# Optimization experiments

Measured on AMD Instinct MI355X. Metric: run time of the kernel, lower is better.

The kernel has to match this reference:

```python
import jax, jax.numpy as jnp
import numpy as np
from jax import lax

B, N, HID = 2, 2048, 2048
H, KVH, D = 16, 4, 128           # heads, kv heads, head_dim
GROUPS = H // KVH
FLA_WEIGHT = 0.01
NEG = -1e30


def setup_inputs() -> dict:
    key = jax.random.key(0)
    ks = jax.random.split(key, 5)
    s = 0.02
    return {
        "hidden_states": jax.random.normal(ks[0], (B, N, HID), jnp.float32),
        "Wq": jax.random.normal(ks[1], (HID, H * D), jnp.float32) * s,
        "Wk": jax.random.normal(ks[2], (HID, KVH * D), jnp.float32) * s,
        "Wv": jax.random.normal(ks[3], (HID, KVH * D), jnp.float32) * s,
        "Wo": jax.random.normal(ks[4], (H * D, HID), jnp.float32) * s,
    }


def _split_heads(x, h):
    b, n, _ = x.shape
    return x.reshape(b, n, h, -1).transpose(0, 2, 1, 3)  # b h n d


def _gla_attention(q, k, v, scale):
    # Gated linear attention: S_t = sigmoid(k_t) (.) S_{t-1} + k_t (x) v_t,
    # o_t = scale * q_t . S_t ; sequential recurrence over the seq dim.
    qs = jnp.moveaxis(q, 2, 0)  # n b h d
    ks = jnp.moveaxis(k, 2, 0)
    vs = jnp.moveaxis(v, 2, 0)

    def step(S, inp):
        qt, kt, vt = inp                                   # each (b,h,d)
        g = jax.nn.sigmoid(kt)                             # per-key-dim gate
        S = S * g[..., None] + kt[..., None] * vt[..., None, :]  # (b,h,d,dv)
        ot = scale * jnp.einsum('bhd,bhde->bhe', qt, S)
        return S, ot

    S0 = jnp.zeros(q.shape[:2] + (q.shape[-1], v.shape[-1]), q.dtype)
    _, o = lax.scan(step, S0, (qs, ks, vs))                # n b h dv
    return jnp.moveaxis(o, 0, 2)                           # b h n dv


def reference(hidden_states, Wq, Wk, Wv, Wo):
    scale = 1.0 / np.sqrt(D)
    q = _split_heads(hidden_states @ Wq, H)                # b h n d
    k = _split_heads(hidden_states @ Wk, KVH)
    v = _split_heads(hidden_states @ Wv, KVH)
    k = jnp.repeat(k, GROUPS, axis=1)                      # repeat_kv -> b H n d
    v = jnp.repeat(v, GROUPS, axis=1)

    # FLA branch
    fla = _gla_attention(q, k, v, scale)                   # b h n d
    fla = fla.transpose(0, 2, 1, 3).reshape(B, N, H * D)   # b n (h d)

    # Base causal softmax attention
    scores = jnp.einsum('bhnd,bhmd->bhnm', q, k) * scale
    causal = jnp.tril(jnp.ones((N, N), bool))
    scores = jnp.where(causal, scores, NEG)
    attn = jax.nn.softmax(scores, axis=-1)
    base = jnp.einsum('bhnm,bhmd->bhnd', attn, v)
    base = base.transpose(0, 2, 1, 3).reshape(B, N, H * D) @ Wo

    return base + FLA_WEIGHT * fla
```

## Files before the change

### kernel.cpp

```cpp
#include <hip/hip_runtime.h>
#include <hip/hip_bf16.h>
#include <cstdint>
#include <cstddef>


typedef __attribute__((ext_vector_type(4))) float f32x4;
typedef __attribute__((ext_vector_type(2))) float f32x2;
typedef __attribute__((ext_vector_type(8))) short s16x8;
typedef unsigned short u16;
typedef unsigned int u32;

__device__ __forceinline__ float bfu2f(u16 u) {
  union { unsigned int i; float f; } x; x.i = ((unsigned int)u) << 16; return x.f;
}
__device__ __forceinline__ u16 f2bfu(float f) {
  union { float f; unsigned int i; } x; x.f = f;
  unsigned int r = x.i + 0x7fffu + ((x.i >> 16) & 1u);
  return (u16)(r >> 16);
}
__device__ __forceinline__ void bf8_to_f(s16x8 v, float* o) {
  union { s16x8 v; u16 u[8]; } x; x.v = v;
#pragma unroll
  for (int j = 0; j < 8; j++) o[j] = bfu2f(x.u[j]);
}
__device__ __forceinline__ s16x8 pack_bf8(f32x4 lo, f32x4 hi) {
  union { s16x8 v; u16 u[8]; } x;
#pragma unroll
  for (int j = 0; j < 4; j++) { x.u[j] = f2bfu(lo[j]); x.u[4 + j] = f2bfu(hi[j]); }
  return x.v;
}
__device__ __forceinline__ void gload_lds16(const u16* g, u16* l) {
  __builtin_amdgcn_global_load_lds(
      (__attribute__((address_space(1))) void*)(g),
      (__attribute__((address_space(3))) void*)(l), 16, 0, 0);
}

__global__ __launch_bounds__(256) void f32_to_bf16(
    const float* __restrict__ src, u16* __restrict__ dst, int n8) {
  const int i = blockIdx.x * 256 + threadIdx.x;
  if (i < n8) {
    f32x4 a = *(const f32x4*)(src + (size_t)i * 8);
    f32x4 b = *(const f32x4*)(src + (size_t)i * 8 + 4);
    *(s16x8*)(dst + (size_t)i * 8) = pack_bf8(a, b);
  }
}

__global__ __launch_bounds__(256) void transpose_f32_bf16(
    const float* __restrict__ src, u16* __restrict__ dst, int R, int C) {
  __shared__ u16 tile[32][33];
  const int bx = blockIdx.x * 32, by = blockIdx.y * 32;
  const int tx = threadIdx.x & 31, ty = threadIdx.x >> 5;
#pragma unroll
  for (int i = 0; i < 32; i += 8)
    tile[ty + i][tx] = f2bfu(src[(size_t)(by + ty + i) * C + bx + tx]);
  __syncthreads();
#pragma unroll
  for (int i = 0; i < 32; i += 8)
    dst[(size_t)(bx + ty + i) * R + by + tx] = tile[tx][ty + i];
}

__global__ __launch_bounds__(256) void transpose_bf16(
    const u16* __restrict__ src, u16* __restrict__ dst, int R, int C) {
  __shared__ u16 tile[32][33];
  const int bx = blockIdx.x * 32, by = blockIdx.y * 32;
  const int tx = threadIdx.x & 31, ty = threadIdx.x >> 5;
#pragma unroll
  for (int i = 0; i < 32; i += 8)
    tile[ty + i][tx] = src[(size_t)(by + ty + i) * C + bx + tx];
  __syncthreads();
#pragma unroll
  for (int i = 0; i < 32; i += 8)
    dst[(size_t)(bx + ty + i) * R + by + tx] = tile[tx][ty + i];
}

__global__ __launch_bounds__(256) void gemm_t(
    const u16* __restrict__ A, const u16* __restrict__ Bt0, const u16* __restrict__ Bt1,
    u16* __restrict__ Cb0, u16* __restrict__ Cb1, float* __restrict__ Cf,
    int M, int N, int K, const u16* __restrict__ addsrc, float addw) {
  __shared__ u16 Al[128 * 32];
  __shared__ u16 Bl[128 * 32];
  const u16* Bt = blockIdx.z ? Bt1 : Bt0;
  u16* Cb = blockIdx.z ? Cb1 : Cb0;
  const int m0 = blockIdx.y * 128, n0 = blockIdx.x * 128;
  const int t = threadIdx.x, w = t >> 6, l = t & 63, lm = l & 15, lq = l >> 4;
  const int wr = w >> 1, wc = w & 1;
  const f32x4 z4 = {0.f, 0.f, 0.f, 0.f};
  f32x4 acc[4][4];
#pragma unroll
  for (int i = 0; i < 4; i++)
#pragma unroll
    for (int j = 0; j < 4; j++) acc[i][j] = z4;
  const int srow = l >> 2, scol = (l & 3) * 8;
  const u16* Ag = A + (size_t)(m0 + w * 32 + srow) * K + scol;
  const u16* Bg = Bt + (size_t)(n0 + w * 32 + srow) * K + scol;
  u16* Alw = &Al[(w * 32) * 32];
  u16* Blw = &Bl[(w * 32) * 32];
  for (int kk = 0; kk < K; kk += 32) {
    gload_lds16(Ag + kk, Alw);
    gload_lds16(Ag + (size_t)16 * K + kk, Alw + 16 * 32);
    gload_lds16(Bg + kk, Blw);
    gload_lds16(Bg + (size_t)16 * K + kk, Blw + 16 * 32);
    __syncthreads();
    s16x8 af[4], bfr[4];
#pragma unroll
    for (int sm = 0; sm < 4; sm++) af[sm] = *(const s16x8*)&Al[(wr * 64 + sm * 16 + lm) * 32 + lq * 8];
#pragma unroll
    for (int sn = 0; sn < 4; sn++) bfr[sn] = *(const s16x8*)&Bl[(wc * 64 + sn * 16 + lm) * 32 + lq * 8];
#pragma unroll
    for (int sm = 0; sm < 4; sm++)
#pragma unroll
      for (int sn = 0; sn < 4; sn++)
        acc[sm][sn] = __builtin_amdgcn_mfma_f32_16x16x32_bf16(af[sm], bfr[sn], acc[sm][sn], 0, 0, 0);
    __syncthreads();
  }
#pragma unroll
  for (int sm = 0; sm < 4; sm++)
#pragma unroll
    for (int sn = 0; sn < 4; sn++)
#pragma unroll
      for (int r = 0; r < 4; r++) {
        const int row = m0 + wr * 64 + sm * 16 + lq * 4 + r;
        const int col = n0 + wc * 64 + sn * 16 + lm;
        float v = acc[sm][sn][r];
        if (Cf) {
          if (addsrc) v += addw * bfu2f(addsrc[(size_t)row * N + col]);
          Cf[(size_t)row * N + col] = v;
        } else {
          Cb[(size_t)row * N + col] = f2bfu(v);
        }
      }
}

__global__ __launch_bounds__(256) void gemm_qkv(
    const u16* __restrict__ A, const u16* __restrict__ WqT, const u16* __restrict__ WkT,
    const u16* __restrict__ WvT, u16* __restrict__ Qo, u16* __restrict__ Ko,
    u16* __restrict__ Vo) {
  __shared__ u16 Al[128 * 32];
  __shared__ u16 Bl[128 * 32];
  const int bx = blockIdx.x;
  const u16* Bt; u16* Cb; int n0, Nst;
  if (bx < 16)      { Bt = WqT; Cb = Qo; n0 = bx * 128;        Nst = 2048; }
  else if (bx < 20) { Bt = WkT; Cb = Ko; n0 = (bx - 16) * 128; Nst = 512; }
  else              { Bt = WvT; Cb = Vo; n0 = (bx - 20) * 128; Nst = 512; }
  const int K = 2048;
  const int m0 = blockIdx.y * 128;
  const int t = threadIdx.x, w = t >> 6, l = t & 63, lm = l & 15, lq = l >> 4;
  const int wr = w >> 1, wc = w & 1;
  const f32x4 z4 = {0.f, 0.f, 0.f, 0.f};
  f32x4 acc[4][4];
#pragma unroll
  for (int i = 0; i < 4; i++)
#pragma unroll
    for (int j = 0; j < 4; j++) acc[i][j] = z4;
  const int srow = l >> 2, scol = (l & 3) * 8;
  const u16* Ag = A + (size_t)(m0 + w * 32 + srow) * K + scol;
  const u16* Bg = Bt + (size_t)(n0 + w * 32 + srow) * K + scol;
  u16* Alw = &Al[(w * 32) * 32];
  u16* Blw = &Bl[(w * 32) * 32];
  for (int kk = 0; kk < K; kk += 32) {
    gload_lds16(Ag + kk, Alw);
    gload_lds16(Ag + (size_t)16 * K + kk, Alw + 16 * 32);
    gload_lds16(Bg + kk, Blw);
    gload_lds16(Bg + (size_t)16 * K + kk, Blw + 16 * 32);
    __syncthreads();
    s16x8 af[4], bfr[4];
#pragma unroll
    for (int sm = 0; sm < 4; sm++) af[sm] = *(const s16x8*)&Al[(wr * 64 + sm * 16 + lm) * 32 + lq * 8];
#pragma unroll
    for (int sn = 0; sn < 4; sn++) bfr[sn] = *(const s16x8*)&Bl[(wc * 64 + sn * 16 + lm) * 32 + lq * 8];
#pragma unroll
    for (int sm = 0; sm < 4; sm++)
#pragma unroll
      for (int sn = 0; sn < 4; sn++)
        acc[sm][sn] = __builtin_amdgcn_mfma_f32_16x16x32_bf16(af[sm], bfr[sn], acc[sm][sn], 0, 0, 0);
    __syncthreads();
  }
#pragma unroll
  for (int sm = 0; sm < 4; sm++)
#pragma unroll
    for (int sn = 0; sn < 4; sn++)
#pragma unroll
      for (int r = 0; r < 4; r++) {
        const int row = m0 + wr * 64 + sm * 16 + lq * 4 + r;
        const int col = n0 + wc * 64 + sn * 16 + lm;
        Cb[(size_t)row * Nst + col] = f2bfu(acc[sm][sn][r]);
      }
}

__global__ __launch_bounds__(512) void flash_attn_wave(
    const u16* __restrict__ Q, const u16* __restrict__ Kx,
    const u16* __restrict__ Vt, u16* __restrict__ AO) {
  __shared__ u16 Klds[2][64 * 128];
  __shared__ u16 Vlds[2][128 * 64];
  __shared__ u16 Pl[8][16][68];
  const int bid = blockIdx.x;
  const int set = bid & 7;
  const int b = set >> 2, kvh = set & 3;
  const int rest = bid >> 3;
  const int j0 = rest >> 1, hp = rest & 1;
  const int t = threadIdx.x, w = t >> 6, l = t & 63, lm = l & 15, lq = l >> 4;
  const int h = kvh * 4 + hp * 2 + (w & 1);
  const int cs = (w >> 1) & 1, mh = w >> 2;
  const float scale = 0.0883883476483184f;
  const u16* Kbase = Kx + (size_t)(b * 2048) * 512 + kvh * 128;
  const u16* Vbase = Vt + (size_t)(b * 512 + kvh * 128) * 2048;
  const f32x4 z4 = {0.f, 0.f, 0.f, 0.f};

  const int kdst0 = w * 512, kdst1 = 4096 + w * 512;
  const int krow_a = (l >> 4), kcol_sw = (((l & 15) * 16)) >> 1;
  (void)krow_a; (void)kcol_sw;

  auto stage = [&](int kt, int bufi) {
    const int key0 = kt * 64;
#pragma unroll
    for (int r = 0; r < 2; r++) {
      const int row = r * 32 + w * 4 + (l >> 4);
      const int scb = ((l & 15) * 16) ^ ((row & 7) << 4);
      gload_lds16(Kbase + (size_t)(key0 + row) * 512 + (scb >> 1),
                  &Klds[bufi][r * 4096 + w * 512]);
    }
#pragma unroll
    for (int r = 0; r < 2; r++) {
      const int row = r * 64 + w * 8 + (l >> 3);
      const int scb = ((l & 7) * 16) ^ ((row & 7) << 4);
      gload_lds16(Vbase + (size_t)row * 2048 + key0 + (scb >> 1),
                  &Vlds[bufi][r * 4096 + w * 512]);
    }
  };

#pragma unroll 1
  for (int ph = 0; ph < 2; ph++) {
    const int j = ph ? (31 - j0) : j0;
    const int c = 2 * j + cs;
    const int base = c * 32;
    int cur = 0;
    stage(0, 0);
    s16x8 qf[4];
#pragma unroll
    for (int kk = 0; kk < 4; kk++)
      qf[kk] = *(const s16x8*)(Q + ((size_t)(b * 2048 + base + mh * 16 + lm)) * 2048 +
                               h * 128 + kk * 32 + lq * 8);
    f32x4 oacc[8];
#pragma unroll
    for (int e = 0; e < 8; e++) oacc[e] = z4;
    float lsum[4] = {0.f, 0.f, 0.f, 0.f};
#pragma unroll 1
    for (int kt = 0; kt <= j; kt++) {
      const int key0 = kt * 64;
      if (kt < j) {
        stage(kt + 1, cur ^ 1);
        asm volatile("s_waitcnt vmcnt(4)" ::: "memory");
      } else {
        asm volatile("s_waitcnt vmcnt(0)" ::: "memory");
      }
      __builtin_amdgcn_s_barrier();
      const char* KB = (const char*)&Klds[cur][0];
      const char* VB = (const char*)&Vlds[cur][0];
      s16x8 kf[4][4];
#pragma unroll
      for (int nst = 0; nst < 4; nst++)
#pragma unroll
        for (int kk = 0; kk < 4; kk++) {
          const int row = nst * 16 + lm;
          const int cb = (kk * 64 + lq * 16) ^ ((row & 7) << 4);
          kf[nst][kk] = *(const s16x8*)(KB + row * 256 + cb);
        }
      f32x4 sacc[4];
#pragma unroll
      for (int i = 0; i < 4; i++) sacc[i] = z4;
#pragma unroll
      for (int nst = 0; nst < 4; nst++)
#pragma unroll
        for (int kk = 0; kk < 4; kk++)
          sacc[nst] = __builtin_amdgcn_mfma_f32_16x16x32_bf16(
              qf[kk], kf[nst][kk], sacc[nst], 0, 0, 0);
      const bool diag = (kt == j);
#pragma unroll
      for (int r = 0; r < 4; r++) {
        const int qrow = base + mh * 16 + lq * 4 + r;
#pragma unroll
        for (int nst = 0; nst < 4; nst++) {
          float pv = __expf(sacc[nst][r] * scale);
          if (diag && (key0 + nst * 16 + lm > qrow)) pv = 0.f;
          lsum[r] += pv;
          Pl[w][lq * 4 + r][nst * 16 + lm] = f2bfu(pv);
        }
      }
      s16x8 vf[8][2];
#pragma unroll
      for (int et = 0; et < 8; et++)
#pragma unroll
        for (int kc = 0; kc < 2; kc++) {
          const int row = et * 16 + lm;
          const int cb = (kc * 64 + lq * 16) ^ ((row & 7) << 4);
          vf[et][kc] = *(const s16x8*)(VB + row * 128 + cb);
        }
      s16x8 pf[2];
#pragma unroll
      for (int kc = 0; kc < 2; kc++)
        pf[kc] = *(const s16x8*)&Pl[w][lm][kc * 32 + lq * 8];
#pragma unroll
      for (int et = 0; et < 8; et++)
#pragma unroll
        for (int kc = 0; kc < 2; kc++)
          oacc[et] = __builtin_amdgcn_mfma_f32_16x16x32_bf16(
              pf[kc], vf[et][kc], oacc[et], 0, 0, 0);
      asm volatile("s_waitcnt lgkmcnt(0)" ::: "memory");
      __builtin_amdgcn_s_barrier();
      cur ^= 1;
    }
#pragma unroll
    for (int r = 0; r < 4; r++) {
#pragma unroll
      for (int off = 1; off < 16; off <<= 1)
        lsum[r] += __shfl_xor(lsum[r], off, 64);
    }
#pragma unroll
    for (int r = 0; r < 4; r++) {
      const float inv = 1.f / lsum[r];
      const int row = base + mh * 16 + lq * 4 + r;
      u16* op = AO + ((size_t)(b * 2048 + row)) * 2048 + h * 128;
#pragma unroll
      for (int et = 0; et < 8; et++) op[et * 16 + lm] = f2bfu(oacc[et][r] * inv);
    }
  }
}

__global__ __launch_bounds__(256) void fla_contrib32(
    const u16* __restrict__ Kx, const u16* __restrict__ Vt,
    u16* __restrict__ Gg, u16* __restrict__ Ktg, u16* __restrict__ MT,
    float* __restrict__ Lam) {
  __shared__ float gl[32][132];
  __shared__ float kl[32][132];
  __shared__ float ktl[32][132];
  __shared__ u16 khT[128][40];
  const int c = blockIdx.x, kvh = blockIdx.y, b = blockIdx.z;
  const int bk = b * 4 + kvh;
  const int t = threadIdx.x;
  const size_t cb = (size_t)bk * 64 + c;
  {
    const int r = t >> 3, c0 = (t & 7) * 16;
    const u16* kp = Kx + ((size_t)(b * 2048 + c * 32 + r)) * 512 + kvh * 128 + c0;
#pragma unroll
    for (int i = 0; i < 2; i++) {
      float kv[8];
      bf8_to_f(*(const s16x8*)(kp + i * 8), kv);
#pragma unroll
      for (int j = 0; j < 8; j++) {
        kl[r][c0 + i * 8 + j] = kv[j];
        gl[r][c0 + i * 8 + j] = 1.f / (1.f + __expf(-kv[j]));
      }
    }
  }
  __syncthreads();
  if (t < 128) {
    float G = 1.f;
#pragma unroll
    for (int s = 0; s < 32; s++) {
      G *= gl[s][t];
      gl[s][t] = G;
      ktl[s][t] = kl[s][t] / G;
    }
    Lam[cb * 128 + t] = G;
    const float lam = G;
#pragma unroll
    for (int s = 0; s < 32; s++) khT[t][s] = f2bfu(ktl[s][t] * lam);
  }
  __syncthreads();
  {
    const int r = t >> 3, c0 = (t & 7) * 16;
    u16* gp = Gg + cb * 4096 + r * 128 + c0;
    u16* kp = Ktg + cb * 4096 + r * 128 + c0;
#pragma unroll
    for (int i = 0; i < 2; i++) {
      f32x4 a = *(f32x4*)&gl[r][c0 + i * 8];
      f32x4 b2 = *(f32x4*)&gl[r][c0 + i * 8 + 4];
      *(s16x8*)(gp + i * 8) = pack_bf8(a, b2);
      a = *(f32x4*)&ktl[r][c0 + i * 8];
      b2 = *(f32x4*)&ktl[r][c0 + i * 8 + 4];
      *(s16x8*)(kp + i * 8) = pack_bf8(a, b2);
    }
  }
  const int w = t >> 6, l = t & 63, lm = l & 15, lq = l >> 4;
  const f32x4 z4 = {0.f, 0.f, 0.f, 0.f};
  f32x4 macc[2][8];
#pragma unroll
  for (int ei = 0; ei < 2; ei++)
#pragma unroll
    for (int dt = 0; dt < 8; dt++) macc[ei][dt] = z4;
  s16x8 vtf[2];
#pragma unroll
  for (int ei = 0; ei < 2; ei++) {
    const int et = w * 2 + ei;
    vtf[ei] = *(const s16x8*)(Vt + ((size_t)(b * 512 + kvh * 128 + et * 16 + lm)) * 2048 +
                              c * 32 + lq * 8);
  }
#pragma unroll
  for (int dt = 0; dt < 8; dt++) {
    s16x8 kf = *(const s16x8*)&khT[dt * 16 + lm][lq * 8];
#pragma unroll
    for (int ei = 0; ei < 2; ei++)
      macc[ei][dt] = __builtin_amdgcn_mfma_f32_16x16x32_bf16(vtf[ei], kf, macc[ei][dt], 0, 0, 0);
  }
  u16* mp = MT + cb * 16384;
#pragma unroll
  for (int ei = 0; ei < 2; ei++)
#pragma unroll
    for (int dt = 0; dt < 8; dt++)
#pragma unroll
      for (int r = 0; r < 4; r++)
        mp[(size_t)((w * 2 + ei) * 16 + lq * 4 + r) * 128 + dt * 16 + lm] =
            f2bfu(macc[ei][dt][r]);
}

__global__ __launch_bounds__(256) void fla_prefix32(
    const u16* __restrict__ MT, const float* __restrict__ Lam, u16* __restrict__ SwsT) {
  const int eg = blockIdx.x, bk = blockIdx.y;
  const int t = threadIdx.x;
  const int e = eg * 4 + (t >> 6), d0 = (t & 63) * 2;
  const size_t cb0 = (size_t)bk * 64;
  const u16* mp = MT + cb0 * 16384 + e * 128 + d0;
  const float* lp = Lam + cb0 * 128 + d0;
  u16* sp = SwsT + cb0 * 16384 + e * 128 + d0;
  float s0 = 0.f, s1 = 0.f;
  u32 mnext = *(const u32*)mp;
  f32x2 lnext = *(const f32x2*)lp;
#pragma unroll 1
  for (int c = 0; c < 64; c++) {
    const u32 mcur = mnext;
    const f32x2 lcur = lnext;
    if (c < 63) {
      mnext = *(const u32*)(mp + (size_t)(c + 1) * 16384);
      lnext = *(const f32x2*)(lp + (size_t)(c + 1) * 128);
    }
    *(u32*)(sp + (size_t)c * 16384) = (u32)f2bfu(s0) | ((u32)f2bfu(s1) << 16);
    s0 = s0 * lcur[0] + bfu2f((u16)(mcur & 0xffffu));
    s1 = s1 * lcur[1] + bfu2f((u16)(mcur >> 16));
  }
}

__global__ __launch_bounds__(256) void fla_output_mfma(
    const u16* __restrict__ Q, const u16* __restrict__ Gg, const u16* __restrict__ Ktg,
    const u16* __restrict__ SwsT, const u16* __restrict__ Vt, u16* __restrict__ Fla) {
  __shared__ u16 Pl[4][2][16][40];
  const int c = blockIdx.x, h = blockIdx.y, b = blockIdx.z;
  const int kvh = h >> 2, bk = b * 4 + kvh;
  const int t = threadIdx.x, w = t >> 6, l = t & 63, lm = l & 15, lq = l >> 4;
  const float scale = 0.0883883476483184f;
  const size_t cb = (size_t)bk * 64 + c;
  const f32x4 z4 = {0.f, 0.f, 0.f, 0.f};
  s16x8 qgf[2][4];
#pragma unroll
  for (int m = 0; m < 2; m++)
#pragma unroll
    for (int kk = 0; kk < 4; kk++) {
      float qv[8], gv[8];
      bf8_to_f(*(const s16x8*)(Q + ((size_t)(b * 2048 + c * 32 + m * 16 + lm)) * 2048 +
                               h * 128 + kk * 32 + lq * 8), qv);
      bf8_to_f(*(const s16x8*)(Gg + cb * 4096 + (m * 16 + lm) * 128 + kk * 32 + lq * 8), gv);
      f32x4 a, b2;
#pragma unroll
      for (int j = 0; j < 4; j++) { a[j] = qv[j] * gv[j]; b2[j] = qv[4 + j] * gv[4 + j]; }
      qgf[m][kk] = pack_bf8(a, b2);
    }
  f32x4 sacc[2][2];
#pragma unroll
  for (int m = 0; m < 2; m++)
#pragma unroll
    for (int st = 0; st < 2; st++) sacc[m][st] = z4;
#pragma unroll
  for (int st = 0; st < 2; st++)
#pragma unroll
    for (int kk = 0; kk < 4; kk++) {
      s16x8 ktf = *(const s16x8*)(Ktg + cb * 4096 + (st * 16 + lm) * 128 + kk * 32 + lq * 8);
#pragma unroll
      for (int m = 0; m < 2; m++)
        sacc[m][st] = __builtin_amdgcn_mfma_f32_16x16x32_bf16(qgf[m][kk], ktf, sacc[m][st], 0, 0, 0);
    }
#pragma unroll
  for (int m = 0; m < 2; m++)
#pragma unroll
    for (int st = 0; st < 2; st++)
#pragma unroll
      for (int r = 0; r < 4; r++) {
        const int trow = m * 16 + lq * 4 + r;
        const int scol = st * 16 + lm;
        Pl[w][m][lq * 4 + r][st * 16 + lm] = f2bfu(scol <= trow ? sacc[m][st][r] : 0.f);
      }
  s16x8 pf[2];
#pragma unroll
  for (int m = 0; m < 2; m++) pf[m] = *(const s16x8*)&Pl[w][m][lm][lq * 8];
  f32x4 oacc[2][2];
#pragma unroll
  for (int m = 0; m < 2; m++)
#pragma unroll
    for (int ei = 0; ei < 2; ei++) oacc[m][ei] = z4;
#pragma unroll
  for (int ei = 0; ei < 2; ei++) {
    const int et = w * 2 + ei;
    s16x8 vtf = *(const s16x8*)(Vt + ((size_t)(b * 512 + kvh * 128 + et * 16 + lm)) * 2048 +
                                c * 32 + lq * 8);
#pragma unroll
    for (int m = 0; m < 2; m++)
      oacc[m][ei] = __builtin_amdgcn_mfma_f32_16x16x32_bf16(pf[m], vtf, oacc[m][ei], 0, 0, 0);
#pragma unroll
    for (int kk = 0; kk < 4; kk++) {
      s16x8 s0f = *(const s16x8*)(SwsT + cb * 16384 + (et * 16 + lm) * 128 + kk * 32 + lq * 8);
#pragma unroll
      for (int m = 0; m < 2; m++)
        oacc[m][ei] = __builtin_amdgcn_mfma_f32_16x16x32_bf16(qgf[m][kk], s0f, oacc[m][ei], 0, 0, 0);
    }
  }
#pragma unroll
  for (int m = 0; m < 2; m++)
#pragma unroll
    for (int ei = 0; ei < 2; ei++)
#pragma unroll
      for (int r = 0; r < 4; r++)
        Fla[((size_t)(b * 2048 + c * 32 + m * 16 + lq * 4 + r)) * 2048 + h * 128 +
            (w * 2 + ei) * 16 + lm] = f2bfu(scale * oacc[m][ei][r]);
}

extern "C" void kernel_launch(void* const* d_in, const int* in_sizes, int n_in,
                              void* d_out, int out_size, void* d_ws, size_t ws_size,
                              hipStream_t stream) {
  const float* X  = (const float*)d_in[0];
  const float* Wq = (const float*)d_in[1];
  const float* Wk = (const float*)d_in[2];
  const float* Wv = (const float*)d_in[3];
  const float* Wo = (const float*)d_in[4];
  float* out = (float*)d_out;

  char* ws = (char*)d_ws;
  size_t off = 0;
  auto alloc = [&](size_t bytes) { void* p = ws + off; off += (bytes + 255) & ~(size_t)255; return p; };
  u16* WoT = (u16*)alloc(2048ull * 2048 * 2);
  u16* Qb  = (u16*)alloc(4096ull * 2048 * 2);
  u16* Kb  = (u16*)alloc(4096ull * 512 * 2);
  u16* Vb  = (u16*)alloc(4096ull * 512 * 2);
  u16* Vtb = (u16*)alloc(2ull * 512 * 2048 * 2);
  u16* Fla = (u16*)alloc(4096ull * 2048 * 2);
  u16* SH16 = (u16*)alloc(4096ull * 2048 * 2);
  u16* Xb = SH16;
  u16* MT = SH16;
  u16* AO = SH16;
  char* BIG = (char*)alloc(26ull * 1024 * 1024);
  u16* WqT = (u16*)BIG;
  u16* WkT = (u16*)(BIG + 8ull * 1024 * 1024);
  u16* WvT = (u16*)(BIG + 10ull * 1024 * 1024);
  u16* Gg   = (u16*)BIG;
  u16* Ktg  = (u16*)(BIG + 4194304ull);
  u16* SwsT = (u16*)(BIG + 8388608ull);
  float* Lam = (float*)(BIG + 8388608ull + 16777216ull);
  (void)ws_size; (void)in_sizes; (void)n_in; (void)out_size;

  dim3 blk(256);
  f32_to_bf16<<<dim3(4096), blk, 0, stream>>>(X, Xb, 4096 * 2048 / 8);
  transpose_f32_bf16<<<dim3(64, 64), blk, 0, stream>>>(Wq, WqT, 2048, 2048);
  transpose_f32_bf16<<<dim3(16, 64), blk, 0, stream>>>(Wk, WkT, 2048, 512);
  transpose_f32_bf16<<<dim3(16, 64), blk, 0, stream>>>(Wv, WvT, 2048, 512);
  transpose_f32_bf16<<<dim3(64, 64), blk, 0, stream>>>(Wo, WoT, 2048, 2048);

  gemm_qkv<<<dim3(24, 32), blk, 0, stream>>>(Xb, WqT, WkT, WvT, Qb, Kb, Vb);

  transpose_bf16<<<dim3(16, 64), blk, 0, stream>>>(Vb, Vtb, 2048, 512);
  transpose_bf16<<<dim3(16, 64), blk, 0, stream>>>(Vb + 2048ull * 512, Vtb + 512ull * 2048, 2048, 512);

  fla_contrib32<<<dim3(64, 4, 2), blk, 0, stream>>>(Kb, Vtb, Gg, Ktg, MT, Lam);
  fla_prefix32<<<dim3(32, 8), blk, 0, stream>>>(MT, Lam, SwsT);
  fla_output_mfma<<<dim3(64, 16, 2), blk, 0, stream>>>(Qb, Gg, Ktg, SwsT, Vtb, Fla);

  flash_attn_wave<<<dim3(256), dim3(512), 0, stream>>>(Qb, Kb, Vtb, AO);

  gemm_t<<<dim3(16, 32, 1), blk, 0, stream>>>(AO, WoT, WoT, nullptr, nullptr, out,
                                              4096, 2048, 2048, Fla, 0.01f);
}
```

Before: 384.7 us.

## Rewrite QKV and output GEMMs with double-buffered 256x128 tiles and swizzled LDS

Result: slower. 396.6 us (+3.1%).

```diff
diff --git a/kernel.cpp b/kernel.cpp
--- a/kernel.cpp
+++ b/kernel.cpp
@@ -73,45 +73,81 @@
     dst[(size_t)(bx + ty + i) * R + by + tx] = tile[tx][ty + i];
 }
 
-__global__ __launch_bounds__(256) void gemm_t(
-    const u16* __restrict__ A, const u16* __restrict__ Bt0, const u16* __restrict__ Bt1,
-    u16* __restrict__ Cb0, u16* __restrict__ Cb1, float* __restrict__ Cf,
-    int M, int N, int K, const u16* __restrict__ addsrc, float addw) {
-  __shared__ u16 Al[128 * 32];
-  __shared__ u16 Bl[128 * 32];
-  const u16* Bt = blockIdx.z ? Bt1 : Bt0;
-  u16* Cb = blockIdx.z ? Cb1 : Cb0;
-  const int m0 = blockIdx.y * 128, n0 = blockIdx.x * 128;
+__device__ __forceinline__ void gemm_core_256x128(
+    const u16* __restrict__ A, const u16* __restrict__ Bt,
+    int m0, int n0, int K, int Nst,
+    u16* __restrict__ Cb, float* __restrict__ Cf,
+    const u16* __restrict__ addsrc, float addw,
+    u16* Abuf, u16* Bbuf) {
   const int t = threadIdx.x, w = t >> 6, l = t & 63, lm = l & 15, lq = l >> 4;
   const int wr = w >> 1, wc = w & 1;
+  const int tr = t >> 3, tc8 = (t & 7) * 8;
   const f32x4 z4 = {0.f, 0.f, 0.f, 0.f};
   f32x4 acc[4][4];
 #pragma unroll
   for (int i = 0; i < 4; i++)
 #pragma unroll
     for (int j = 0; j < 4; j++) acc[i][j] = z4;
-  const int srow = l >> 2, scol = (l & 3) * 8;
-  const u16* Ag = A + (size_t)(m0 + w * 32 + srow) * K + scol;
-  const u16* Bg = Bt + (size_t)(n0 + w * 32 + srow) * K + scol;
-  u16* Alw = &Al[(w * 32) * 32];
-  u16* Blw = &Bl[(w * 32) * 32];
-  for (int kk = 0; kk < K; kk += 32) {
-    gload_lds16(Ag + kk, Alw);
-    gload_lds16(Ag + (size_t)16 * K + kk, Alw + 16 * 32);
-    gload_lds16(Bg + kk, Blw);
-    gload_lds16(Bg + (size_t)16 * K + kk, Blw + 16 * 32);
-    __syncthreads();
-    s16x8 af[4], bfr[4];
-#pragma unroll
-    for (int sm = 0; sm < 4; sm++) af[sm] = *(const s16x8*)&Al[(wr * 64 + sm * 16 + lm) * 32 + lq * 8];
-#pragma unroll
-    for (int sn = 0; sn < 4; sn++) bfr[sn] = *(const s16x8*)&Bl[(wc * 64 + sn * 16 + lm) * 32 + lq * 8];
-#pragma unroll
-    for (int sm = 0; sm < 4; sm++)
-#pragma unroll
-      for (int sn = 0; sn < 4; sn++)
-        acc[sm][sn] = __builtin_amdgcn_mfma_f32_16x16x32_bf16(af[sm], bfr[sn], acc[sm][sn], 0, 0, 0);
-    __syncthreads();
+  const u16* Ag = A + (size_t)m0 * K;
+  const u16* Bg = Bt + (size_t)n0 * K;
+  auto stage = [&](int kt, int bufi) {
+#pragma unroll
+    for (int i = 0; i < 4; i++) {
+      const int row = i * 64 + tr;
+      const int col = tc8 ^ ((row & 7) << 3);
+      gload_lds16(Ag + (size_t)row * K + kt * 64 + col,
+                  Abuf + bufi * 16384 + i * 4096 + w * 512);
+    }
+#pragma unroll
+    for (int i = 0; i < 2; i++) {
+      const int row = i * 64 + tr;
+      const int col = tc8 ^ ((row & 7) << 3);
+      gload_lds16(Bg + (size_t)row * K + kt * 64 + col,
+                  Bbuf + bufi * 8192 + i * 4096 + w * 512);
+    }
+  };
+  const int nt = K >> 6;
+  stage(0, 0);
+  int cur = 0;
+#pragma unroll 1
+  for (int kt = 0; kt < nt; kt++) {
+    if (kt + 1 < nt) {
+      stage(kt + 1, cur ^ 1);
+      asm volatile("s_waitcnt vmcnt(6)" ::: "memory");
+    } else {
+      asm volatile("s_waitcnt vmcnt(0)" ::: "memory");
+    }
+    __builtin_amdgcn_s_barrier();
+    const u16* Ab = Abuf + cur * 16384;
+    const u16* Bb = Bbuf + cur * 8192;
+    s16x8 af[4][2], bff[4][2];
+#pragma unroll
+    for (int sm = 0; sm < 4; sm++) {
+      const int row = wr * 64 + sm * 16 + lm;
+#pragma unroll
+      for (int kk = 0; kk < 2; kk++)
+        af[sm][kk] = *(const s16x8*)&Ab[row * 64 +
+            ((((kk << 6) | (lq << 4)) ^ ((row & 7) << 4)) >> 1)];
+    }
+#pragma unroll
+    for (int sn = 0; sn < 4; sn++) {
+      const int row = wc * 64 + sn * 16 + lm;
+#pragma unroll
+      for (int kk = 0; kk < 2; kk++)
+        bff[sn][kk] = *(const s16x8*)&Bb[row * 64 +
+            ((((kk << 6) | (lq << 4)) ^ ((row & 7) << 4)) >> 1)];
+    }
+#pragma unroll
+    for (int kk = 0; kk < 2; kk++)
+#pragma unroll
+      for (int sm = 0; sm < 4; sm++)
+#pragma unroll
+        for (int sn = 0; sn < 4; sn++)
+          acc[sm][sn] = __builtin_amdgcn_mfma_f32_16x16x32_bf16(
+              af[sm][kk], bff[sn][kk], acc[sm][sn], 0, 0, 0);
+    asm volatile("s_waitcnt lgkmcnt(0)" ::: "memory");
+    __builtin_amdgcn_s_barrier();
+    cur ^= 1;
   }
 #pragma unroll
   for (int sm = 0; sm < 4; sm++)
@@ -123,68 +159,41 @@
         const int col = n0 + wc * 64 + sn * 16 + lm;
         float v = acc[sm][sn][r];
         if (Cf) {
-          if (addsrc) v += addw * bfu2f(addsrc[(size_t)row * N + col]);
-          Cf[(size_t)row * N + col] = v;
+          if (addsrc) v += addw * bfu2f(addsrc[(size_t)row * Nst + col]);
+          Cf[(size_t)row * Nst + col] = v;
         } else {
-          Cb[(size_t)row * N + col] = f2bfu(v);
+          Cb[(size_t)row * Nst + col] = f2bfu(v);
         }
       }
 }
 
-__global__ __launch_bounds__(256) void gemm_qkv(
+__global__ __launch_bounds__(512) void gemm_qkv2(
     const u16* __restrict__ A, const u16* __restrict__ WqT, const u16* __restrict__ WkT,
     const u16* __restrict__ WvT, u16* __restrict__ Qo, u16* __restrict__ Ko,
     u16* __restrict__ Vo) {
-  __shared__ u16 Al[128 * 32];
-  __shared__ u16 Bl[128 * 32];
-  const int bx = blockIdx.x;
+  __shared__ u16 Abuf[2 * 16384];
+  __shared__ u16 Bbuf[2 * 8192];
+  int f = blockIdx.y * 24 + blockIdx.x;
+  f = (f & 7) * 48 + (f >> 3);
+  const int by = f / 24, bx = f - by * 24;
   const u16* Bt; u16* Cb; int n0, Nst;
   if (bx < 16)      { Bt = WqT; Cb = Qo; n0 = bx * 128;        Nst = 2048; }
   else if (bx < 20) { Bt = WkT; Cb = Ko; n0 = (bx - 16) * 128; Nst = 512; }
   else              { Bt = WvT; Cb = Vo; n0 = (bx - 20) * 128; Nst = 512; }
-  const int K = 2048;
-  const int m0 = blockIdx.y * 128;
-  const int t = threadIdx.x, w = t >> 6, l = t & 63, lm = l & 15, lq = l >> 4;
-  const int wr = w >> 1, wc = w & 1;
-  const f32x4 z4 = {0.f, 0.f, 0.f, 0.f};
-  f32x4 acc[4][4];
-#pragma unroll
-  for (int i = 0; i < 4; i++)
-#pragma unroll
-    for (int j = 0; j < 4; j++) acc[i][j] = z4;
-  const int srow = l >> 2, scol = (l & 3) * 8;
-  const u16* Ag = A + (size_t)(m0 + w * 32 + srow) * K + scol;
-  const u16* Bg = Bt + (size_t)(n0 + w * 32 + srow) * K + scol;
-  u16* Alw = &Al[(w * 32) * 32];
-  u16* Blw = &Bl[(w * 32) * 32];
-  for (int kk = 0; kk < K; kk += 32) {
-    gload_lds16(Ag + kk, Alw);
-    gload_lds16(Ag + (size_t)16 * K + kk, Alw + 16 * 32);
-    gload_lds16(Bg + kk, Blw);
-    gload_lds16(Bg + (size_t)16 * K + kk, Blw + 16 * 32);
-    __syncthreads();
-    s16x8 af[4], bfr[4];
-#pragma unroll
-    for (int sm = 0; sm < 4; sm++) af[sm] = *(const s16x8*)&Al[(wr * 64 + sm * 16 + lm) * 32 + lq * 8];
-#pragma unroll
-    for (int sn = 0; sn < 4; sn++) bfr[sn] = *(const s16x8*)&Bl[(wc * 64 + sn * 16 + lm) * 32 + lq * 8];
-#pragma unroll
-    for (int sm = 0; sm < 4; sm++)
-#pragma unroll
-      for (int sn = 0; sn < 4; sn++)
-        acc[sm][sn] = __builtin_amdgcn_mfma_f32_16x16x32_bf16(af[sm], bfr[sn], acc[sm][sn], 0, 0, 0);
-    __syncthreads();
-  }
-#pragma unroll
-  for (int sm = 0; sm < 4; sm++)
-#pragma unroll
-    for (int sn = 0; sn < 4; sn++)
-#pragma unroll
-      for (int r = 0; r < 4; r++) {
-        const int row = m0 + wr * 64 + sm * 16 + lq * 4 + r;
-        const int col = n0 + wc * 64 + sn * 16 + lm;
-        Cb[(size_t)row * Nst + col] = f2bfu(acc[sm][sn][r]);
-      }
+  gemm_core_256x128(A, Bt, by * 256, n0, 2048, Nst, Cb, nullptr, nullptr, 0.f,
+                    Abuf, Bbuf);
+}
+
+__global__ __launch_bounds__(512) void gemm_out2(
+    const u16* __restrict__ A, const u16* __restrict__ Bt, float* __restrict__ Cf,
+    const u16* __restrict__ addsrc) {
+  __shared__ u16 Abuf[2 * 16384];
+  __shared__ u16 Bbuf[2 * 8192];
+  int f = blockIdx.y * 16 + blockIdx.x;
+  f = (f & 7) * 32 + (f >> 3);
+  const int by = f >> 4, bx = f & 15;
+  gemm_core_256x128(A, Bt, by * 256, bx * 128, 2048, 2048, nullptr, Cf,
+                    addsrc, 0.01f, Abuf, Bbuf);
 }
 
 __global__ __launch_bounds__(512) void flash_attn_wave(
@@ -205,10 +214,6 @@
   const u16* Kbase = Kx + (size_t)(b * 2048) * 512 + kvh * 128;
   const u16* Vbase = Vt + (size_t)(b * 512 + kvh * 128) * 2048;
   const f32x4 z4 = {0.f, 0.f, 0.f, 0.f};
-
-  const int kdst0 = w * 512, kdst1 = 4096 + w * 512;
-  const int krow_a = (l >> 4), kcol_sw = (((l & 15) * 16)) >> 1;
-  (void)krow_a; (void)kcol_sw;
 
   auto stage = [&](int kt, int bufi) {
     const int key0 = kt * 64;
@@ -561,7 +566,7 @@
   transpose_f32_bf16<<<dim3(16, 64), blk, 0, stream>>>(Wv, WvT, 2048, 512);
   transpose_f32_bf16<<<dim3(64, 64), blk, 0, stream>>>(Wo, WoT, 2048, 2048);
 
-  gemm_qkv<<<dim3(24, 32), blk, 0, stream>>>(Xb, WqT, WkT, WvT, Qb, Kb, Vb);
+  gemm_qkv2<<<dim3(24, 16), dim3(512), 0, stream>>>(Xb, WqT, WkT, WvT, Qb, Kb, Vb);
 
   transpose_bf16<<<dim3(16, 64), blk, 0, stream>>>(Vb, Vtb, 2048, 512);
   transpose_bf16<<<dim3(16, 64), blk, 0, stream>>>(Vb + 2048ull * 512, Vtb + 512ull * 2048, 2048, 512);
@@ -572,6 +577,5 @@
 
   flash_attn_wave<<<dim3(256), dim3(512), 0, stream>>>(Qb, Kb, Vtb, AO);
 
-  gemm_t<<<dim3(16, 32, 1), blk, 0, stream>>>(AO, WoT, WoT, nullptr, nullptr, out,
-                                              4096, 2048, 2048, Fla, 0.01f);
-}
+  gemm_out2<<<dim3(16, 16), dim3(512), 0, stream>>>(AO, WoT, out, Fla);
+}
```
